# Kernel optimization log

Hardware: AMD Instinct MI355X
Metric: run time of the kernel (lower is better)

## Reference

```python
import jax, jax.numpy as jnp
import numpy as np

D_MODEL = 1024
NUM_HEADS = 16
DEPTH = D_MODEL // NUM_HEADS  # 64
B, S = 4, 2048
NEG_BIG = -1000000000.0


def setup_inputs() -> dict:
    key = jax.random.key(0)
    ks = jax.random.split(key, 9)
    # Glorot-uniform per-head projection weights, stacked over heads: [H, d_model, depth]
    lim_qkv = np.sqrt(6.0 / (D_MODEL + DEPTH)).astype(np.float32)
    lim_o = np.sqrt(6.0 / (D_MODEL + D_MODEL)).astype(np.float32)
    x = jax.random.normal(ks[0], (B, S, D_MODEL), dtype=jnp.float32)
    attention_mask = jnp.ones((B, S, 1), dtype=jnp.float32)
    Wq = jax.random.uniform(ks[1], (NUM_HEADS, D_MODEL, DEPTH), jnp.float32, -lim_qkv, lim_qkv)
    Wk = jax.random.uniform(ks[2], (NUM_HEADS, D_MODEL, DEPTH), jnp.float32, -lim_qkv, lim_qkv)
    Wv = jax.random.uniform(ks[3], (NUM_HEADS, D_MODEL, DEPTH), jnp.float32, -lim_qkv, lim_qkv)
    bq = jnp.zeros((NUM_HEADS, DEPTH), jnp.float32)
    bk = jnp.zeros((NUM_HEADS, DEPTH), jnp.float32)
    bv = jnp.zeros((NUM_HEADS, DEPTH), jnp.float32)
    Wo = jax.random.uniform(ks[4], (D_MODEL, D_MODEL), jnp.float32, -lim_o, lim_o)
    bo = jnp.zeros((D_MODEL,), jnp.float32)
    return {"x": x, "attention_mask": attention_mask, "Wq": Wq, "bq": bq,
            "Wk": Wk, "bk": bk, "Wv": Wv, "bv": bv, "Wo": Wo, "bo": bo}


def reference(x, attention_mask, Wq, bq, Wk, bk, Wv, bv, Wo, bo):
    # Batched over heads (same math as the per-head Python loop + concat).
    # x: [B,S,D]; Wq/Wk/Wv: [H,D,depth]; bq/bk/bv: [H,depth]
    q = jnp.einsum('bsd,hde->bhse', x, Wq) + bq[None, :, None, :]
    k = jnp.einsum('bsd,hde->bhse', x, Wk) + bk[None, :, None, :]
    v = jnp.einsum('bsd,hde->bhse', x, Wv) + bv[None, :, None, :]
    scale = 1.0 / jnp.sqrt(jnp.asarray(DEPTH, dtype=x.dtype))
    scores = jnp.einsum('bhse,bhte->bhst', q, k) * scale  # [B,H,S,S]
    # original: mask.transpose(-2,-1) -> [B,1,S], broadcast over query rows; add head axis
    mask_t = jnp.swapaxes(attention_mask, -2, -1)[:, None]  # [B,1,1,S]
    scores = scores + (1.0 - mask_t) * NEG_BIG
    probs = jax.nn.softmax(scores, axis=-1)
    z = jnp.einsum('bhst,bhte->bhse', probs, v)  # [B,H,S,depth]
    # concat heads along feature dim (head order matches torch.cat order)
    multi_head = jnp.transpose(z, (0, 2, 1, 3)).reshape(x.shape[0], x.shape[1], NUM_HEADS * DEPTH)
    return multi_head @ Wo + bo
```

## Files before the change

### kernel.cpp

```cpp
#include <hip/hip_runtime.h>

#define NH 16
#define DEP 64
#define DM 1024
#define BB 4
#define SS 2048

typedef __attribute__((ext_vector_type(8))) __bf16 bf16x8;
typedef __attribute__((ext_vector_type(4))) __bf16 bf16x4;
typedef __attribute__((ext_vector_type(2))) __bf16 bf16x2;
typedef __attribute__((ext_vector_type(4))) float f32x4;
typedef __attribute__((ext_vector_type(4))) unsigned u32x4;
typedef __attribute__((ext_vector_type(2))) unsigned u32x2;
typedef unsigned short u16;

#define MFMA_BF16(A, B, C) __builtin_amdgcn_mfma_f32_16x16x32_bf16(A, B, C, 0, 0, 0)

#define SCL 0.18033688011112042f
#define LOG2E 1.4426950408889634f

__device__ __forceinline__ u16 f2bf(float f) {
  unsigned u = __builtin_bit_cast(unsigned, f);
  u += 0x7fffu + ((u >> 16) & 1u);
  return (u16)(u >> 16);
}

__device__ __forceinline__ unsigned pk2(float a, float b) {
  bf16x2 t;
  t[0] = (__bf16)a; t[1] = (__bf16)b;
  return __builtin_bit_cast(unsigned, t);
}

__device__ __forceinline__ void gload_lds16(const u16* g, u16* l) {
  __builtin_amdgcn_global_load_lds((const __attribute__((address_space(1))) void*)g,
                                   (__attribute__((address_space(3))) void*)l, 16, 0, 0);
}

__global__ __launch_bounds__(256) void k_cvt_x(const float* __restrict__ x, u16* __restrict__ xb) {
  int i = (blockIdx.x * 256 + threadIdx.x) * 4;
  float4 v = *(const float4*)(x + i);
  ushort4 o;
  o.x = f2bf(v.x); o.y = f2bf(v.y); o.z = f2bf(v.z); o.w = f2bf(v.w);
  *(ushort4*)(xb + i) = o;
}

__global__ __launch_bounds__(256) void k_pack_qkv(const float* __restrict__ Wq, const float* __restrict__ Wk,
                                                  const float* __restrict__ Wv,
                                                  const float* __restrict__ bq, const float* __restrict__ bk,
                                                  const float* __restrict__ bv,
                                                  u16* __restrict__ wt, float* __restrict__ biasN) {
  __shared__ float lt[64][65];
  int k0 = blockIdx.x * 64;
  int z = blockIdx.y;
  int which = z >> 4, h = z & 15;
  const float* W = which == 0 ? Wq : (which == 1 ? Wk : Wv);
  const float* bsrc = which == 0 ? bq : (which == 1 ? bk : bv);
  const float* src = W + (size_t)h * DM * DEP;
  int t = threadIdx.x;
#pragma unroll
  for (int p = 0; p < 16; ++p) {
    int li = p * 256 + t;
    int r = li >> 6, c = li & 63;
    lt[r][c] = src[(size_t)(k0 + r) * 64 + c];
  }
  __syncthreads();
  int woff = which * DM + h * 64;
#pragma unroll
  for (int p = 0; p < 16; ++p) {
    int li = p * 256 + t;
    int r = li >> 6, c = li & 63;
    wt[(size_t)(woff + r) * DM + k0 + c] = f2bf(lt[c][r]);
  }
  if (blockIdx.x == 0 && t < 64) biasN[woff + t] = bsrc[h * 64 + t];
}

__global__ __launch_bounds__(256) void k_pack_wo(const float* __restrict__ Wo, u16* __restrict__ wot) {
  __shared__ float lt[64][65];
  int k0 = blockIdx.x * 64, n0 = blockIdx.y * 64;
  int t = threadIdx.x;
#pragma unroll
  for (int p = 0; p < 16; ++p) {
    int li = p * 256 + t;
    int r = li >> 6, c = li & 63;
    lt[r][c] = Wo[(size_t)(k0 + r) * DM + n0 + c];
  }
  __syncthreads();
#pragma unroll
  for (int p = 0; p < 16; ++p) {
    int li = p * 256 + t;
    int r = li >> 6, c = li & 63;
    wot[(size_t)(n0 + r) * DM + k0 + c] = f2bf(lt[c][r]);
  }
}

__global__ __launch_bounds__(256) void k_maskbias(const float* __restrict__ mask, float* __restrict__ mb) {
  int i = blockIdx.x * 256 + threadIdx.x;
  mb[i] = (1.0f - mask[i]) * (-1000000000.0f * LOG2E);
}

__global__ __launch_bounds__(256) void k_gemm_qkv(const u16* __restrict__ xb, const u16* __restrict__ wt,
                                                  const float* __restrict__ biasN,
                                                  u16* __restrict__ qb, u16* __restrict__ kb,
                                                  u16* __restrict__ vtb) {
  __shared__ u16 lA[2][128 * 32];
  __shared__ u16 lB[2][128 * 32];
  const int tid = threadIdx.x;
  const int lane = tid & 63, w = tid >> 6;
  const int m0 = blockIdx.x * 128, n0 = blockIdx.y * 128;
  const int wm = (w >> 1) * 64, wn = (w & 1) * 64;
  const int fr = lane & 15, fg = lane >> 4;
  const int bidx = tid * 16;
  const int row0 = bidx >> 6, c0 = (bidx & 63) >> 1;
  f32x4 acc[4][4] = {};
  auto stage = [&](int k0, int buf) {
    gload_lds16(xb + (size_t)(m0 + row0) * DM + k0 + c0, &lA[buf][w * 512]);
    gload_lds16(xb + (size_t)(m0 + row0 + 64) * DM + k0 + c0, &lA[buf][2048 + w * 512]);
    gload_lds16(wt + (size_t)(n0 + row0) * DM + k0 + c0, &lB[buf][w * 512]);
    gload_lds16(wt + (size_t)(n0 + row0 + 64) * DM + k0 + c0, &lB[buf][2048 + w * 512]);
  };
  stage(0, 0);
  __syncthreads();
  for (int k0 = 0; k0 < DM; k0 += 32) {
    const int cur = (k0 >> 5) & 1;
    if (k0 + 32 < DM) stage(k0 + 32, cur ^ 1);
    bf16x8 af[4], bfr[4];
#pragma unroll
    for (int i = 0; i < 4; ++i) {
      af[i] = *(const bf16x8*)&lA[cur][(wm + i * 16 + fr) * 32 + fg * 8];
      bfr[i] = *(const bf16x8*)&lB[cur][(wn + i * 16 + fr) * 32 + fg * 8];
    }
#pragma unroll
    for (int i = 0; i < 4; ++i)
#pragma unroll
      for (int j = 0; j < 4; ++j)
        acc[i][j] = MFMA_BF16(af[i], bfr[j], acc[i][j]);
    __syncthreads();
  }
#pragma unroll
  for (int i = 0; i < 4; ++i)
#pragma unroll
    for (int j = 0; j < 4; ++j) {
      int n = n0 + wn + j * 16 + fr;
      float bn = biasN[n];
      int which = n >> 10, rem = n & 1023, h = rem >> 6, d = rem & 63;
#pragma unroll
      for (int r = 0; r < 4; ++r) {
        int m = m0 + wm + i * 16 + fg * 4 + r;
        int b = m >> 11, s = m & 2047;
        float val = acc[i][j][r] + bn;
        if (which == 0)      qb[(((size_t)(b * NH + h) * SS + s) << 6) + d] = f2bf(val * SCL);
        else if (which == 1) kb[(((size_t)(b * NH + h) * SS + s) << 6) + d] = f2bf(val);
        else                 vtb[(((size_t)(b * NH + h) * 64 + d) << 11) + s] = f2bf(val);
      }
    }
}

__global__ __launch_bounds__(256, 2) void k_attn(const u16* __restrict__ qb, const u16* __restrict__ kb,
                                                 const u16* __restrict__ vtb, const float* __restrict__ mbias,
                                                 u16* __restrict__ zb) {
  __shared__ u16 sK[2][64 * 64];
  __shared__ u16 sV[2][64 * 64];
  const int bh = blockIdx.y;
  const int b = bh >> 4, h = bh & 15;
  const int tid = threadIdx.x, lane = tid & 63, w = tid >> 6;
  const int q0 = blockIdx.x * 256 + w * 64;
  const u16* Q  = qb  + (size_t)bh * SS * 64;
  const u16* K  = kb  + (size_t)bh * SS * 64;
  const u16* VT = vtb + (size_t)bh * 64 * SS;
  const float* mbb = mbias + b * SS;
  const int fr = lane & 15, fg = lane >> 4;
  const int fr7 = fr & 7;
  const int rsub = lane >> 3;
  const int cg = (lane & 7) ^ rsub;
  const int kc0 = (fg ^ fr7) * 16;
  const int kc1 = ((4 + fg) ^ fr7) * 16;
  const int fg1 = fg >> 1, fgb = (fg & 1) * 8;
  const int cX0 = (((fg1)     ^ fr7)) * 16 + fgb;
  const int cX1 = (((2 + (fg1 ^ 1)) ^ fr7)) * 16 + fgb;
  const int cY0 = (((4 + fg1) ^ fr7)) * 16 + fgb;
  const int cY1 = (((6 + (fg1 ^ 1)) ^ fr7)) * 16 + fgb;
  bf16x8 qlo[4], qhi[4];
#pragma unroll
  for (int qf = 0; qf < 4; ++qf) {
    qlo[qf] = *(const bf16x8*)&Q[(q0 + 16 * qf + fr) * 64 + fg * 8];
    qhi[qf] = *(const bf16x8*)&Q[(q0 + 16 * qf + fr) * 64 + 32 + fg * 8];
  }
  float lrun[4] = {0.f, 0.f, 0.f, 0.f};
  f32x4 o[4][4] = {};

#pragma unroll
  for (int j = 0; j < 2; ++j) {
    int i = w * 2 + j;
    gload_lds16(K + (size_t)(8 * i + rsub) * 64 + cg * 8, &sK[0][i * 512]);
    gload_lds16(VT + (size_t)(8 * i + rsub) * SS + cg * 8, &sV[0][i * 512]);
  }
  __syncthreads();

  for (int t = 0; t < 32; ++t) {
    const int cur = t & 1;
    if (t < 31) {
      const int kvn = (t + 1) * 64;
#pragma unroll
      for (int j = 0; j < 2; ++j) {
        int i = w * 2 + j;
        gload_lds16(K + (size_t)(kvn + 8 * i + rsub) * 64 + cg * 8, &sK[cur ^ 1][i * 512]);
        gload_lds16(VT + (size_t)(8 * i + rsub) * SS + kvn + cg * 8, &sV[cur ^ 1][i * 512]);
      }
    }
    const int kv = t * 64;
    const char* Kb = (const char*)&sK[cur][0];
    const char* Vb = (const char*)&sV[cur][0];
    bf16x8 klo[4], khi[4];
#pragma unroll
    for (int kt = 0; kt < 4; ++kt) {
      klo[kt] = *(const bf16x8*)(Kb + (kt * 16 + fr) * 128 + kc0);
      khi[kt] = *(const bf16x8*)(Kb + (kt * 16 + fr) * 128 + kc1);
    }
    u32x2 vx0[4], vx1[4], vy0[4], vy1[4];
#pragma unroll
    for (int dc = 0; dc < 4; ++dc) {
      const char* rb = Vb + (dc * 16 + fr) * 128;
      vx0[dc] = *(const u32x2*)(rb + cX0);
      vx1[dc] = *(const u32x2*)(rb + cX1);
      vy0[dc] = *(const u32x2*)(rb + cY0);
      vy1[dc] = *(const u32x2*)(rb + cY1);
    }
#pragma unroll
    for (int qf = 0; qf < 4; ++qf) {
      f32x4 sc[4];
      __builtin_amdgcn_s_setprio(1);
#pragma unroll
      for (int kt = 0; kt < 4; ++kt) {
        f32x4 mb4 = *(const f32x4*)(mbb + kv + kt * 16 + fg * 4);
        sc[kt] = MFMA_BF16(khi[kt], qhi[qf], MFMA_BF16(klo[kt], qlo[qf], mb4));
      }
      __builtin_amdgcn_s_setprio(0);
      float e00 = __builtin_amdgcn_exp2f(sc[0][0]), e01 = __builtin_amdgcn_exp2f(sc[0][1]);
      float e02 = __builtin_amdgcn_exp2f(sc[0][2]), e03 = __builtin_amdgcn_exp2f(sc[0][3]);
      float e10 = __builtin_amdgcn_exp2f(sc[1][0]), e11 = __builtin_amdgcn_exp2f(sc[1][1]);
      float e12 = __builtin_amdgcn_exp2f(sc[1][2]), e13 = __builtin_amdgcn_exp2f(sc[1][3]);
      float e20 = __builtin_amdgcn_exp2f(sc[2][0]), e21 = __builtin_amdgcn_exp2f(sc[2][1]);
      float e22 = __builtin_amdgcn_exp2f(sc[2][2]), e23 = __builtin_amdgcn_exp2f(sc[2][3]);
      float e30 = __builtin_amdgcn_exp2f(sc[3][0]), e31 = __builtin_amdgcn_exp2f(sc[3][1]);
      float e32 = __builtin_amdgcn_exp2f(sc[3][2]), e33 = __builtin_amdgcn_exp2f(sc[3][3]);
      lrun[qf] += ((e00 + e01) + (e02 + e03)) + ((e10 + e11) + (e12 + e13))
                + ((e20 + e21) + (e22 + e23)) + ((e30 + e31) + (e32 + e33));
      unsigned w00 = pk2(e00, e01), w01 = pk2(e02, e03);
      unsigned w10 = pk2(e10, e11), w11 = pk2(e12, e13);
      unsigned w20 = pk2(e20, e21), w21 = pk2(e22, e23);
      unsigned w30 = pk2(e30, e31), w31 = pk2(e32, e33);
      unsigned x2 = (unsigned)__shfl_xor((int)w10, 32);
      unsigned x3 = (unsigned)__shfl_xor((int)w11, 32);
      unsigned y2 = (unsigned)__shfl_xor((int)w30, 32);
      unsigned y3 = (unsigned)__shfl_xor((int)w31, 32);
      u32x4 ux = {w00, w01, x2, x3};
      u32x4 uy = {w20, w21, y2, y3};
      bf16x8 paX = __builtin_bit_cast(bf16x8, ux);
      bf16x8 paY = __builtin_bit_cast(bf16x8, uy);
      __builtin_amdgcn_s_setprio(1);
#pragma unroll
      for (int dc = 0; dc < 4; ++dc) {
        u32x4 vxw = {vx0[dc][0], vx0[dc][1], vx1[dc][0], vx1[dc][1]};
        u32x4 vyw = {vy0[dc][0], vy0[dc][1], vy1[dc][0], vy1[dc][1]};
        bf16x8 vX = __builtin_bit_cast(bf16x8, vxw);
        bf16x8 vY = __builtin_bit_cast(bf16x8, vyw);
        o[qf][dc] = MFMA_BF16(paX, vX, o[qf][dc]);
        o[qf][dc] = MFMA_BF16(paY, vY, o[qf][dc]);
      }
      __builtin_amdgcn_s_setprio(0);
    }
    __syncthreads();
  }
#pragma unroll
  for (int qf = 0; qf < 4; ++qf) {
    float l = lrun[qf];
    l += __shfl_xor(l, 16);
    l += __shfl_xor(l, 32);
#pragma unroll
    for (int r = 0; r < 4; ++r) {
      float linv = 1.0f / __shfl(l, 4 * fg + r);
      int s = q0 + 16 * qf + 4 * fg + r;
#pragma unroll
      for (int dc = 0; dc < 4; ++dc)
        zb[(size_t)(b * SS + s) * DM + h * 64 + dc * 16 + fr] = f2bf(o[qf][dc][r] * linv);
    }
  }
}

__global__ __launch_bounds__(256) void k_gemm_out(const u16* __restrict__ zb, const u16* __restrict__ wot,
                                                  const float* __restrict__ bo, float* __restrict__ out) {
  __shared__ u16 lA[2][128 * 32];
  __shared__ u16 lB[2][128 * 32];
  const int tid = threadIdx.x;
  const int lane = tid & 63, w = tid >> 6;
  const int m0 = blockIdx.x * 128, n0 = blockIdx.y * 128;
  const int wm = (w >> 1) * 64, wn = (w & 1) * 64;
  const int fr = lane & 15, fg = lane >> 4;
  const int bidx = tid * 16;
  const int row0 = bidx >> 6, c0 = (bidx & 63) >> 1;
  f32x4 acc[4][4] = {};
  auto stage = [&](int k0, int buf) {
    gload_lds16(zb + (size_t)(m0 + row0) * DM + k0 + c0, &lA[buf][w * 512]);
    gload_lds16(zb + (size_t)(m0 + row0 + 64) * DM + k0 + c0, &lA[buf][2048 + w * 512]);
    gload_lds16(wot + (size_t)(n0 + row0) * DM + k0 + c0, &lB[buf][w * 512]);
    gload_lds16(wot + (size_t)(n0 + row0 + 64) * DM + k0 + c0, &lB[buf][2048 + w * 512]);
  };
  stage(0, 0);
  __syncthreads();
  for (int k0 = 0; k0 < DM; k0 += 32) {
    const int cur = (k0 >> 5) & 1;
    if (k0 + 32 < DM) stage(k0 + 32, cur ^ 1);
    bf16x8 af[4], bfr[4];
#pragma unroll
    for (int i = 0; i < 4; ++i) {
      af[i] = *(const bf16x8*)&lA[cur][(wm + i * 16 + fr) * 32 + fg * 8];
      bfr[i] = *(const bf16x8*)&lB[cur][(wn + i * 16 + fr) * 32 + fg * 8];
    }
#pragma unroll
    for (int i = 0; i < 4; ++i)
#pragma unroll
      for (int j = 0; j < 4; ++j)
        acc[i][j] = MFMA_BF16(af[i], bfr[j], acc[i][j]);
    __syncthreads();
  }
#pragma unroll
  for (int i = 0; i < 4; ++i)
#pragma unroll
    for (int j = 0; j < 4; ++j) {
      int n = n0 + wn + j * 16 + fr;
      float bn = bo[n];
#pragma unroll
      for (int r = 0; r < 4; ++r) {
        int m = m0 + wm + i * 16 + fg * 4 + r;
        out[(size_t)m * DM + n] = acc[i][j][r] + bn;
      }
    }
}

extern "C" void kernel_launch(void* const* d_in, const int* in_sizes, int n_in,
                              void* d_out, int out_size, void* d_ws, size_t ws_size,
                              hipStream_t stream) {
  const float* x    = (const float*)d_in[0];
  const float* mask = (const float*)d_in[1];
  const float* Wq   = (const float*)d_in[2];
  const float* bq   = (const float*)d_in[3];
  const float* Wk   = (const float*)d_in[4];
  const float* bk   = (const float*)d_in[5];
  const float* Wv   = (const float*)d_in[6];
  const float* bv   = (const float*)d_in[7];
  const float* Wo   = (const float*)d_in[8];
  const float* bo   = (const float*)d_in[9];
  char* ws = (char*)d_ws;
  u16*   xb    = (u16*)(ws + 0);
  u16*   zb    = xb;
  u16*   wt    = (u16*)(ws + 16777216);
  u16*   wot   = (u16*)(ws + 23068672);
  float* biasN = (float*)(ws + 25165824);
  float* mb    = (float*)(ws + 25178112);
  u16*   qb    = (u16*)(ws + 25210880);
  u16*   kb    = (u16*)(ws + 41988096);
  u16*   vtb   = (u16*)(ws + 58765312);
  float* out   = (float*)d_out;

  k_cvt_x<<<dim3(8192), dim3(256), 0, stream>>>(x, xb);
  k_pack_qkv<<<dim3(16, 48), dim3(256), 0, stream>>>(Wq, Wk, Wv, bq, bk, bv, wt, biasN);
  k_pack_wo<<<dim3(16, 16), dim3(256), 0, stream>>>(Wo, wot);
  k_maskbias<<<dim3(32), dim3(256), 0, stream>>>(mask, mb);
  k_gemm_qkv<<<dim3(64, 24), dim3(256), 0, stream>>>(xb, wt, biasN, qb, kb, vtb);
  k_attn<<<dim3(8, 64), dim3(256), 0, stream>>>(qb, kb, vtb, mb, zb);
  k_gemm_out<<<dim3(64, 8), dim3(256), 0, stream>>>(zb, wot, bo, out);
}
```

Baseline: 218.1 us.

## Load K/V directly from global in attention, drop LDS staging and barriers

The attention kernel no longer stages K and V tiles through double-buffered shared memory with per-tile __syncthreads. Each wave now reads its K fragments and transposed-V fragments straight from global memory, relying on L2/L1 for sharing. K for the next 32-key step is register double-buffered, and the key step shrinks from 64 to 32. The grid becomes 1D with a block-index swizzle that spreads consecutive blocks across heads, which changes how blocks land on CUs and in cache. This removes LDS traffic and barriers at the cost of redundant global loads across the four waves and smaller per-iteration MFMA batches.

```diff
diff --git a/kernel.cpp b/kernel.cpp
--- a/kernel.cpp
+++ b/kernel.cpp
@@ -7,7 +7,6 @@
 #define SS 2048
 
 typedef __attribute__((ext_vector_type(8))) __bf16 bf16x8;
-typedef __attribute__((ext_vector_type(4))) __bf16 bf16x4;
 typedef __attribute__((ext_vector_type(2))) __bf16 bf16x2;
 typedef __attribute__((ext_vector_type(4))) float f32x4;
 typedef __attribute__((ext_vector_type(4))) unsigned u32x4;
@@ -158,27 +157,19 @@
 __global__ __launch_bounds__(256, 2) void k_attn(const u16* __restrict__ qb, const u16* __restrict__ kb,
                                                  const u16* __restrict__ vtb, const float* __restrict__ mbias,
                                                  u16* __restrict__ zb) {
-  __shared__ u16 sK[2][64 * 64];
-  __shared__ u16 sV[2][64 * 64];
-  const int bh = blockIdx.y;
+  const int bid = blockIdx.x;
+  const int sw = (bid & 7) * 64 + (bid >> 3);
+  const int bh = sw >> 3;
+  const int qx = sw & 7;
   const int b = bh >> 4, h = bh & 15;
   const int tid = threadIdx.x, lane = tid & 63, w = tid >> 6;
-  const int q0 = blockIdx.x * 256 + w * 64;
+  const int q0 = qx * 256 + w * 64;
   const u16* Q  = qb  + (size_t)bh * SS * 64;
   const u16* K  = kb  + (size_t)bh * SS * 64;
   const u16* VT = vtb + (size_t)bh * 64 * SS;
   const float* mbb = mbias + b * SS;
   const int fr = lane & 15, fg = lane >> 4;
-  const int fr7 = fr & 7;
-  const int rsub = lane >> 3;
-  const int cg = (lane & 7) ^ rsub;
-  const int kc0 = (fg ^ fr7) * 16;
-  const int kc1 = ((4 + fg) ^ fr7) * 16;
-  const int fg1 = fg >> 1, fgb = (fg & 1) * 8;
-  const int cX0 = (((fg1)     ^ fr7)) * 16 + fgb;
-  const int cX1 = (((2 + (fg1 ^ 1)) ^ fr7)) * 16 + fgb;
-  const int cY0 = (((4 + fg1) ^ fr7)) * 16 + fgb;
-  const int cY1 = (((6 + (fg1 ^ 1)) ^ fr7)) * 16 + fgb;
+  const int fgx = fg ^ 2;
   bf16x8 qlo[4], qhi[4];
 #pragma unroll
   for (int qf = 0; qf < 4; ++qf) {
@@ -187,90 +178,78 @@
   }
   float lrun[4] = {0.f, 0.f, 0.f, 0.f};
   f32x4 o[4][4] = {};
-
-#pragma unroll
-  for (int j = 0; j < 2; ++j) {
-    int i = w * 2 + j;
-    gload_lds16(K + (size_t)(8 * i + rsub) * 64 + cg * 8, &sK[0][i * 512]);
-    gload_lds16(VT + (size_t)(8 * i + rsub) * SS + cg * 8, &sV[0][i * 512]);
-  }
-  __syncthreads();
-
-  for (int t = 0; t < 32; ++t) {
-    const int cur = t & 1;
-    if (t < 31) {
-      const int kvn = (t + 1) * 64;
-#pragma unroll
-      for (int j = 0; j < 2; ++j) {
-        int i = w * 2 + j;
-        gload_lds16(K + (size_t)(kvn + 8 * i + rsub) * 64 + cg * 8, &sK[cur ^ 1][i * 512]);
-        gload_lds16(VT + (size_t)(8 * i + rsub) * SS + kvn + cg * 8, &sV[cur ^ 1][i * 512]);
-      }
-    }
-    const int kv = t * 64;
-    const char* Kb = (const char*)&sK[cur][0];
-    const char* Vb = (const char*)&sV[cur][0];
-    bf16x8 klo[4], khi[4];
-#pragma unroll
-    for (int kt = 0; kt < 4; ++kt) {
-      klo[kt] = *(const bf16x8*)(Kb + (kt * 16 + fr) * 128 + kc0);
-      khi[kt] = *(const bf16x8*)(Kb + (kt * 16 + fr) * 128 + kc1);
-    }
-    u32x2 vx0[4], vx1[4], vy0[4], vy1[4];
-#pragma unroll
-    for (int dc = 0; dc < 4; ++dc) {
-      const char* rb = Vb + (dc * 16 + fr) * 128;
-      vx0[dc] = *(const u32x2*)(rb + cX0);
-      vx1[dc] = *(const u32x2*)(rb + cX1);
-      vy0[dc] = *(const u32x2*)(rb + cY0);
-      vy1[dc] = *(const u32x2*)(rb + cY1);
-    }
+  const u16* Kp  = K + fr * 64 + fg * 8;
+  const u16* Vr0 = VT + (size_t)(fr)      * SS;
+  const u16* Vr1 = VT + (size_t)(16 + fr) * SS;
+  const u16* Vr2 = VT + (size_t)(32 + fr) * SS;
+  const u16* Vr3 = VT + (size_t)(48 + fr) * SS;
+
+  bf16x8 ka0, ka1, ka2, ka3, kb0_, kb1_, kb2_, kb3_;
+  ka0 = *(const bf16x8*)(Kp);
+  ka1 = *(const bf16x8*)(Kp + 32);
+  ka2 = *(const bf16x8*)(Kp + 16 * 64);
+  ka3 = *(const bf16x8*)(Kp + 16 * 64 + 32);
+  Kp += 32 * 64;
+
+  auto body = [&](int t, bf16x8& c0, bf16x8& c1, bf16x8& c2, bf16x8& c3,
+                  bf16x8& n0, bf16x8& n1, bf16x8& n2, bf16x8& n3) {
+    const int kv = t * 32;
+    u32x2 va0 = *(const u32x2*)(Vr0 + kv + 4 * fg);
+    u32x2 vb0 = *(const u32x2*)(Vr0 + kv + 16 + 4 * fgx);
+    u32x2 va1 = *(const u32x2*)(Vr1 + kv + 4 * fg);
+    u32x2 vb1 = *(const u32x2*)(Vr1 + kv + 16 + 4 * fgx);
+    u32x2 va2 = *(const u32x2*)(Vr2 + kv + 4 * fg);
+    u32x2 vb2 = *(const u32x2*)(Vr2 + kv + 16 + 4 * fgx);
+    u32x2 va3 = *(const u32x2*)(Vr3 + kv + 4 * fg);
+    u32x2 vb3 = *(const u32x2*)(Vr3 + kv + 16 + 4 * fgx);
+    if (t < 63) {
+      n0 = *(const bf16x8*)(Kp);
+      n1 = *(const bf16x8*)(Kp + 32);
+      n2 = *(const bf16x8*)(Kp + 16 * 64);
+      n3 = *(const bf16x8*)(Kp + 16 * 64 + 32);
+      Kp += 32 * 64;
+    }
+    f32x4 mb0 = *(const f32x4*)(mbb + kv + 4 * fg);
+    f32x4 mb1 = *(const f32x4*)(mbb + kv + 16 + 4 * fg);
+    u32x4 uv0 = {va0[0], va0[1], vb0[0], vb0[1]};
+    u32x4 uv1 = {va1[0], va1[1], vb1[0], vb1[1]};
+    u32x4 uv2 = {va2[0], va2[1], vb2[0], vb2[1]};
+    u32x4 uv3 = {va3[0], va3[1], vb3[0], vb3[1]};
+    bf16x8 v0 = __builtin_bit_cast(bf16x8, uv0);
+    bf16x8 v1 = __builtin_bit_cast(bf16x8, uv1);
+    bf16x8 v2 = __builtin_bit_cast(bf16x8, uv2);
+    bf16x8 v3 = __builtin_bit_cast(bf16x8, uv3);
 #pragma unroll
     for (int qf = 0; qf < 4; ++qf) {
-      f32x4 sc[4];
       __builtin_amdgcn_s_setprio(1);
-#pragma unroll
-      for (int kt = 0; kt < 4; ++kt) {
-        f32x4 mb4 = *(const f32x4*)(mbb + kv + kt * 16 + fg * 4);
-        sc[kt] = MFMA_BF16(khi[kt], qhi[qf], MFMA_BF16(klo[kt], qlo[qf], mb4));
-      }
+      f32x4 s0 = MFMA_BF16(c1, qhi[qf], MFMA_BF16(c0, qlo[qf], mb0));
+      f32x4 s1 = MFMA_BF16(c3, qhi[qf], MFMA_BF16(c2, qlo[qf], mb1));
       __builtin_amdgcn_s_setprio(0);
-      float e00 = __builtin_amdgcn_exp2f(sc[0][0]), e01 = __builtin_amdgcn_exp2f(sc[0][1]);
-      float e02 = __builtin_amdgcn_exp2f(sc[0][2]), e03 = __builtin_amdgcn_exp2f(sc[0][3]);
-      float e10 = __builtin_amdgcn_exp2f(sc[1][0]), e11 = __builtin_amdgcn_exp2f(sc[1][1]);
-      float e12 = __builtin_amdgcn_exp2f(sc[1][2]), e13 = __builtin_amdgcn_exp2f(sc[1][3]);
-      float e20 = __builtin_amdgcn_exp2f(sc[2][0]), e21 = __builtin_amdgcn_exp2f(sc[2][1]);
-      float e22 = __builtin_amdgcn_exp2f(sc[2][2]), e23 = __builtin_amdgcn_exp2f(sc[2][3]);
-      float e30 = __builtin_amdgcn_exp2f(sc[3][0]), e31 = __builtin_amdgcn_exp2f(sc[3][1]);
-      float e32 = __builtin_amdgcn_exp2f(sc[3][2]), e33 = __builtin_amdgcn_exp2f(sc[3][3]);
-      lrun[qf] += ((e00 + e01) + (e02 + e03)) + ((e10 + e11) + (e12 + e13))
-                + ((e20 + e21) + (e22 + e23)) + ((e30 + e31) + (e32 + e33));
+      float e00 = __builtin_amdgcn_exp2f(s0[0]), e01 = __builtin_amdgcn_exp2f(s0[1]);
+      float e02 = __builtin_amdgcn_exp2f(s0[2]), e03 = __builtin_amdgcn_exp2f(s0[3]);
+      float e10 = __builtin_amdgcn_exp2f(s1[0]), e11 = __builtin_amdgcn_exp2f(s1[1]);
+      float e12 = __builtin_amdgcn_exp2f(s1[2]), e13 = __builtin_amdgcn_exp2f(s1[3]);
+      lrun[qf] += ((e00 + e01) + (e02 + e03)) + ((e10 + e11) + (e12 + e13));
       unsigned w00 = pk2(e00, e01), w01 = pk2(e02, e03);
       unsigned w10 = pk2(e10, e11), w11 = pk2(e12, e13);
-      unsigned w20 = pk2(e20, e21), w21 = pk2(e22, e23);
-      unsigned w30 = pk2(e30, e31), w31 = pk2(e32, e33);
       unsigned x2 = (unsigned)__shfl_xor((int)w10, 32);
       unsigned x3 = (unsigned)__shfl_xor((int)w11, 32);
-      unsigned y2 = (unsigned)__shfl_xor((int)w30, 32);
-      unsigned y3 = (unsigned)__shfl_xor((int)w31, 32);
       u32x4 ux = {w00, w01, x2, x3};
-      u32x4 uy = {w20, w21, y2, y3};
       bf16x8 paX = __builtin_bit_cast(bf16x8, ux);
-      bf16x8 paY = __builtin_bit_cast(bf16x8, uy);
       __builtin_amdgcn_s_setprio(1);
-#pragma unroll
-      for (int dc = 0; dc < 4; ++dc) {
-        u32x4 vxw = {vx0[dc][0], vx0[dc][1], vx1[dc][0], vx1[dc][1]};
-        u32x4 vyw = {vy0[dc][0], vy0[dc][1], vy1[dc][0], vy1[dc][1]};
-        bf16x8 vX = __builtin_bit_cast(bf16x8, vxw);
-        bf16x8 vY = __builtin_bit_cast(bf16x8, vyw);
-        o[qf][dc] = MFMA_BF16(paX, vX, o[qf][dc]);
-        o[qf][dc] = MFMA_BF16(paY, vY, o[qf][dc]);
-      }
+      o[qf][0] = MFMA_BF16(paX, v0, o[qf][0]);
+      o[qf][1] = MFMA_BF16(paX, v1, o[qf][1]);
+      o[qf][2] = MFMA_BF16(paX, v2, o[qf][2]);
+      o[qf][3] = MFMA_BF16(paX, v3, o[qf][3]);
       __builtin_amdgcn_s_setprio(0);
     }
-    __syncthreads();
-  }
+  };
+
+  for (int tt = 0; tt < 64; tt += 2) {
+    body(tt,     ka0, ka1, ka2, ka3, kb0_, kb1_, kb2_, kb3_);
+    body(tt + 1, kb0_, kb1_, kb2_, kb3_, ka0, ka1, ka2, ka3);
+  }
+
 #pragma unroll
   for (int qf = 0; qf < 4; ++qf) {
     float l = lrun[qf];
@@ -367,6 +346,6 @@
   k_pack_wo<<<dim3(16, 16), dim3(256), 0, stream>>>(Wo, wot);
   k_maskbias<<<dim3(32), dim3(256), 0, stream>>>(mask, mb);
   k_gemm_qkv<<<dim3(64, 24), dim3(256), 0, stream>>>(xb, wt, biasN, qb, kb, vtb);
-  k_attn<<<dim3(8, 64), dim3(256), 0, stream>>>(qb, kb, vtb, mb, zb);
+  k_attn<<<dim3(512), dim3(256), 0, stream>>>(qb, kb, vtb, mb, zb);
   k_gemm_out<<<dim3(64, 8), dim3(256), 0, stream>>>(zb, wot, bo, out);
 }
```

Measured after the change: 310.9 us. 1.43x slower.
